# Kernel optimization log

Measured on AMD Instinct MI355X. Metric: run time of the kernel, lower is better.

The kernel has to match this reference:

```python
import jax, jax.numpy as jnp
import numpy as np

TEMPERATURE = 2.0  # registered buffer in the torch module
TAU = 1.0
N_HEADS = 16


def setup_inputs() -> dict:
    key = jax.random.key(0)
    ks = jax.random.split(key, 8)
    B, S, D, N = 4, 1024, 1024, 4096
    scale = 1.0 / np.sqrt(D)
    return {
        "x": jax.random.normal(ks[0], (B, S, D), jnp.float32),
        "in_proj_w": jax.random.normal(ks[1], (3 * D, D), jnp.float32) * scale,
        "in_proj_b": jnp.zeros((3 * D,), jnp.float32),
        "out_w": jax.random.normal(ks[2], (D, D), jnp.float32) * scale,
        "out_b": jnp.zeros((D,), jnp.float32),
        "aff_w": jax.random.normal(ks[3], (N, D), jnp.float32) * scale,
        "aff_b": jnp.zeros((N,), jnp.float32),
        "k": 256,
    }


def _forward(x, in_proj_w, in_proj_b, out_w, out_b, aff_w, aff_b, k):
    B, S, D = x.shape
    H = N_HEADS
    hd = D // H
    # packed QKV projection (torch nn.MultiheadAttention layout)
    qkv = x @ in_proj_w.T + in_proj_b                      # [B,S,3D]
    q, kk, v = jnp.split(qkv, 3, axis=-1)
    q = q.reshape(B, S, H, hd).transpose(0, 2, 1, 3)       # [B,H,S,hd]
    kk = kk.reshape(B, S, H, hd).transpose(0, 2, 1, 3)
    v = v.reshape(B, S, H, hd).transpose(0, 2, 1, 3)
    scores = jnp.einsum("bhqd,bhkd->bhqk", q, kk) / np.sqrt(hd)
    attn = jax.nn.softmax(scores, axis=-1)                 # [B,H,S,S]
    ctx = jnp.einsum("bhqk,bhkd->bhqd", attn, v)
    ctx = ctx.transpose(0, 2, 1, 3).reshape(B, S, D)
    context = ctx @ out_w.T + out_b                        # [B,S,D]
    # neuron affinity -> max-pool over sequence
    affinity = context @ aff_w.T + aff_b                   # [B,S,N]
    pooled = affinity.max(axis=1)                          # [B,N]
    logits = pooled / TEMPERATURE
    # eval path of gumbel-softmax-topk: plain softmax(logits / tau)
    soft = jax.nn.softmax(logits / TAU, axis=-1)
    _, idx = jax.lax.top_k(logits, k)                      # [B,k]
    mask = jnp.zeros_like(soft).at[jnp.arange(soft.shape[0])[:, None], idx].set(1.0)
    masked = soft * mask
    weights = masked / (masked.sum(axis=-1, keepdims=True) + 1e-8)
    return idx, weights, context


def reference(x, in_proj_w, in_proj_b, out_w, out_b, aff_w, aff_b, k):
    return _forward(x, in_proj_w, in_proj_b, out_w, out_b, aff_w, aff_b, k)
```

## Files before the change

kernel.cpp:

```cpp
#include <hip/hip_runtime.h>
#include <math.h>

namespace {

constexpr int Bb = 4, Ss = 1024, Dd = 1024, Hh = 16, HDim = 64, Nn = 4096;
constexpr int Mm = Bb * Ss;

__device__ inline void gload_lds16(const void* g, void* l) {
  __builtin_amdgcn_global_load_lds(
      (const __attribute__((address_space(1))) void*)g,
      (__attribute__((address_space(3))) void*)l, 16, 0, 0);
}

template <int MODE, int TM>
__global__ __launch_bounds__(256, 2) void gemm_f32(
    const float* __restrict__ A, const float* __restrict__ W,
    const float* __restrict__ bias, float* __restrict__ C, const int K,
    const int ldc) {
  constexpr int BM = TM * 16;
  __shared__ float As[2][16][BM];
  __shared__ float Ws[2][16][128];
  __shared__ float red[2][128];
  const int tid = threadIdx.x;
  const int lane = tid & 63, wv = tid >> 6;
  const int wm = wv >> 1, wn = wv & 1;
  const int lty = lane >> 3, ltx = lane & 7;
  const int m0 = blockIdx.y * BM, n0 = blockIdx.x * 128;
  const int row0 = wm * (BM / 2) + lty * TM;
  const int col0 = wn * 64 + ltx * 8;
  const int asrow = (TM == 8) ? (tid >> 1) : (tid >> 2);
  const int asoff = (TM == 8) ? ((tid & 1) * 8) : ((tid & 3) * 4);
  const int bsrow = tid >> 1, bsoff = (tid & 1) * 8;
  const float* Ap = A + (size_t)(m0 + asrow) * K + asoff;
  const float* Wp = W + (size_t)(n0 + bsrow) * K + bsoff;

  float4 a0r, a1r, w0r, w1r;
  a0r = *(const float4*)(Ap);
  if constexpr (TM == 8) a1r = *(const float4*)(Ap + 4);
  w0r = *(const float4*)(Wp);
  w1r = *(const float4*)(Wp + 4);

  float acc[TM][8] = {};
  const int NT = K / 16;
#pragma unroll 1
  for (int kt = 0; kt < NT; ++kt) {
    float* Ab = &As[kt & 1][0][0];
    float* Wb = &Ws[kt & 1][0][0];
    Ab[(asoff + 0) * BM + asrow] = a0r.x;
    Ab[(asoff + 1) * BM + asrow] = a0r.y;
    Ab[(asoff + 2) * BM + asrow] = a0r.z;
    Ab[(asoff + 3) * BM + asrow] = a0r.w;
    if constexpr (TM == 8) {
      Ab[(asoff + 4) * BM + asrow] = a1r.x;
      Ab[(asoff + 5) * BM + asrow] = a1r.y;
      Ab[(asoff + 6) * BM + asrow] = a1r.z;
      Ab[(asoff + 7) * BM + asrow] = a1r.w;
    }
    Wb[(bsoff + 0) * 128 + bsrow] = w0r.x;
    Wb[(bsoff + 1) * 128 + bsrow] = w0r.y;
    Wb[(bsoff + 2) * 128 + bsrow] = w0r.z;
    Wb[(bsoff + 3) * 128 + bsrow] = w0r.w;
    Wb[(bsoff + 4) * 128 + bsrow] = w1r.x;
    Wb[(bsoff + 5) * 128 + bsrow] = w1r.y;
    Wb[(bsoff + 6) * 128 + bsrow] = w1r.z;
    Wb[(bsoff + 7) * 128 + bsrow] = w1r.w;
    __syncthreads();
    if (kt + 1 < NT) {
      const int kb = (kt + 1) * 16;
      a0r = *(const float4*)(Ap + kb);
      if constexpr (TM == 8) a1r = *(const float4*)(Ap + kb + 4);
      w0r = *(const float4*)(Wp + kb);
      w1r = *(const float4*)(Wp + kb + 4);
    }
#pragma unroll
    for (int kk = 0; kk < 16; ++kk) {
      float4 aq0 = *(const float4*)&Ab[kk * BM + row0];
      float4 aq1;
      if constexpr (TM == 8) aq1 = *(const float4*)&Ab[kk * BM + row0 + 4];
      float4 bq0 = *(const float4*)&Wb[kk * 128 + col0];
      float4 bq1 = *(const float4*)&Wb[kk * 128 + col0 + 4];
      float av[TM];
      av[0] = aq0.x; av[1] = aq0.y; av[2] = aq0.z; av[3] = aq0.w;
      if constexpr (TM == 8) {
        av[4] = aq1.x; av[5] = aq1.y; av[6] = aq1.z; av[7] = aq1.w;
      }
      const float bv[8] = {bq0.x, bq0.y, bq0.z, bq0.w,
                           bq1.x, bq1.y, bq1.z, bq1.w};
#pragma unroll
      for (int i = 0; i < TM; ++i)
#pragma unroll
        for (int j = 0; j < 8; ++j)
          acc[i][j] = fmaf(av[i], bv[j], acc[i][j]);
    }
  }

  if constexpr (MODE == 0) {
    float4 bb0 = *(const float4*)&bias[n0 + col0];
    float4 bb1 = *(const float4*)&bias[n0 + col0 + 4];
    const float bvv[8] = {bb0.x, bb0.y, bb0.z, bb0.w,
                          bb1.x, bb1.y, bb1.z, bb1.w};
#pragma unroll
    for (int i = 0; i < TM; ++i) {
      float* crow = C + (size_t)(m0 + row0 + i) * ldc + n0 + col0;
      float4 o0 = {acc[i][0] + bvv[0], acc[i][1] + bvv[1],
                   acc[i][2] + bvv[2], acc[i][3] + bvv[3]};
      float4 o1 = {acc[i][4] + bvv[4], acc[i][5] + bvv[5],
                   acc[i][6] + bvv[6], acc[i][7] + bvv[7]};
      *(float4*)(crow) = o0;
      *(float4*)(crow + 4) = o1;
    }
  } else {
    float cm[8];
#pragma unroll
    for (int j = 0; j < 8; ++j) {
      float m = acc[0][j];
#pragma unroll
      for (int i = 1; i < TM; ++i) m = fmaxf(m, acc[i][j]);
      m = fmaxf(m, __shfl_xor(m, 8));
      m = fmaxf(m, __shfl_xor(m, 16));
      m = fmaxf(m, __shfl_xor(m, 32));
      cm[j] = m;
    }
    __syncthreads();
    if (lty == 0) {
      float4 c0 = {cm[0], cm[1], cm[2], cm[3]};
      float4 c1 = {cm[4], cm[5], cm[6], cm[7]};
      *(float4*)&red[wm][wn * 64 + ltx * 8] = c0;
      *(float4*)&red[wm][wn * 64 + ltx * 8 + 4] = c1;
    }
    __syncthreads();
    if (tid < 128)
      C[(size_t)blockIdx.y * ldc + n0 + tid] =
          fmaxf(red[0][tid], red[1][tid]);
  }
}

__device__ __forceinline__ int kkey(int r) { return ((r >> 3) ^ r) & 7; }
__device__ __forceinline__ int swz(int r, int c) { return c ^ (kkey(r) << 2); }
__device__ __forceinline__ int swzp(int r, int c) {
  return c ^ ((kkey(r) & 3) << 2);
}

__global__ __launch_bounds__(256, 2) void attn_kernel(
    const float* __restrict__ qkv, float* __restrict__ ctx) {
  __shared__ float Qs[4][32][64];
  __shared__ float Ks[2][16][64];
  __shared__ float Vs[2][16][64];
  __shared__ float Pw[4][32][16];
  const int tid = threadIdx.x, wv = tid >> 6, lane = tid & 63;
  const int rg = lane >> 3, cg = lane & 7;
  const int id = blockIdx.x;
  const int qb = id >> 6, bh = id & 63;
  const int b = bh >> 4, h = bh & 15;
  const int q0 = qb * 128 + wv * 32;
  const size_t rstride = 3 * Dd;
  const float* qbp = qkv + (size_t)b * Ss * rstride + h * HDim;
  const float* kbp = qbp + Dd;
  const float* vbp = qbp + 2 * Dd;

  {
    const int r = lane >> 1, ch = (lane & 1) * 32;
    const float* qr = qbp + (size_t)(q0 + r) * rstride + ch;
#pragma unroll
    for (int c = 0; c < 32; c += 4)
      *(float4*)&Qs[wv][r][swz(r, ch + c)] = *(const float4*)(qr + c);
  }

  const int srow = lane >> 4;
  const int scol = (lane & 15) * 4;
#define STAGE_KV(KT, BF)                                                      \
  {                                                                           \
    _Pragma("unroll") for (int j = 0; j < 2; ++j) {                           \
      const int g = wv * 2 + j;                                               \
      const int rr = (g & 3) * 4 + srow;                                      \
      const int cc = swz(rr, scol);                                           \
      if (g < 4)                                                              \
        gload_lds16(kbp + (size_t)((KT) + rr) * rstride + cc,                 \
                    &Ks[BF][(g & 3) * 4][0]);                                 \
      else                                                                    \
        gload_lds16(vbp + (size_t)((KT) + rr) * rstride + cc,                 \
                    &Vs[BF][(g & 3) * 4][0]);                                 \
    }                                                                         \
  }

  STAGE_KV(0, 0);
  __syncthreads();

  float O[4][8] = {};
  float mr[4], lr[4];
#pragma unroll
  for (int i = 0; i < 4; ++i) { mr[i] = -INFINITY; lr[i] = 0.f; }

#pragma unroll 1
  for (int t = 0; t < Ss / 16; ++t) {
    const int cur = t & 1;
    if (t + 1 < Ss / 16) STAGE_KV((t + 1) * 16, cur ^ 1);
    float sc[4][2] = {};
#pragma unroll
    for (int d0 = 0; d0 < HDim; d0 += 4) {
      float4 qa[4], kv[2];
#pragma unroll
      for (int i = 0; i < 4; ++i) {
        const int r = rg * 4 + i;
        qa[i] = *(const float4*)&Qs[wv][r][swz(r, d0)];
      }
#pragma unroll
      for (int j = 0; j < 2; ++j) {
        const int r = cg * 2 + j;
        kv[j] = *(const float4*)&Ks[cur][r][swz(r, d0)];
      }
#pragma unroll
      for (int i = 0; i < 4; ++i)
#pragma unroll
        for (int j = 0; j < 2; ++j) {
          sc[i][j] = fmaf(qa[i].x, kv[j].x, sc[i][j]);
          sc[i][j] = fmaf(qa[i].y, kv[j].y, sc[i][j]);
          sc[i][j] = fmaf(qa[i].z, kv[j].z, sc[i][j]);
          sc[i][j] = fmaf(qa[i].w, kv[j].w, sc[i][j]);
        }
    }
#pragma unroll
    for (int i = 0; i < 4; ++i) {
      const float s0 = sc[i][0] * 0.125f, s1 = sc[i][1] * 0.125f;
      float tm = fmaxf(s0, s1);
      tm = fmaxf(tm, __shfl_xor(tm, 1));
      tm = fmaxf(tm, __shfl_xor(tm, 2));
      tm = fmaxf(tm, __shfl_xor(tm, 4));
      const float mnew = fmaxf(mr[i], tm);
      const float p0 = __expf(s0 - mnew), p1 = __expf(s1 - mnew);
      float rs = p0 + p1;
      rs += __shfl_xor(rs, 1);
      rs += __shfl_xor(rs, 2);
      rs += __shfl_xor(rs, 4);
      const float corr = __expf(mr[i] - mnew);
      lr[i] = lr[i] * corr + rs;
      mr[i] = mnew;
#pragma unroll
      for (int c = 0; c < 8; ++c) O[i][c] *= corr;
      const int r = rg * 4 + i;
      float2 pv = {p0, p1};
      *(float2*)&Pw[wv][r][swzp(r, cg * 2)] = pv;
    }
#pragma unroll
    for (int k0 = 0; k0 < 16; k0 += 4) {
      float4 pa[4];
#pragma unroll
      for (int i = 0; i < 4; ++i) {
        const int r = rg * 4 + i;
        pa[i] = *(const float4*)&Pw[wv][r][swzp(r, k0)];
      }
#pragma unroll
      for (int jj = 0; jj < 4; ++jj) {
        const int vr = k0 + jj;
        const float4 v0 = *(const float4*)&Vs[cur][vr][swz(vr, cg * 8)];
        const float4 v1 = *(const float4*)&Vs[cur][vr][swz(vr, cg * 8 + 4)];
#pragma unroll
        for (int i = 0; i < 4; ++i) {
          const float p = (jj == 0) ? pa[i].x
                          : (jj == 1) ? pa[i].y
                          : (jj == 2) ? pa[i].z : pa[i].w;
          O[i][0] = fmaf(p, v0.x, O[i][0]);
          O[i][1] = fmaf(p, v0.y, O[i][1]);
          O[i][2] = fmaf(p, v0.z, O[i][2]);
          O[i][3] = fmaf(p, v0.w, O[i][3]);
          O[i][4] = fmaf(p, v1.x, O[i][4]);
          O[i][5] = fmaf(p, v1.y, O[i][5]);
          O[i][6] = fmaf(p, v1.z, O[i][6]);
          O[i][7] = fmaf(p, v1.w, O[i][7]);
        }
      }
    }
    __syncthreads();
  }
#pragma unroll
  for (int i = 0; i < 4; ++i) {
    const float inv = 1.0f / lr[i];
    float* orow =
        ctx + ((size_t)(b * Ss + q0 + rg * 4 + i)) * Dd + h * HDim + cg * 8;
    float4 o0 = {O[i][0] * inv, O[i][1] * inv, O[i][2] * inv, O[i][3] * inv};
    float4 o1 = {O[i][4] * inv, O[i][5] * inv, O[i][6] * inv, O[i][7] * inv};
    *(float4*)(orow) = o0;
    *(float4*)(orow + 4) = o1;
  }
#undef STAGE_KV
}

__device__ inline unsigned int f2s(float f) {
  unsigned int u = __float_as_uint(f);
  return (u >> 31) ? ~u : (u | 0x80000000u);
}
__device__ inline float s2f(unsigned int s) {
  unsigned int u = (s >> 31) ? (s & 0x7fffffffu) : ~s;
  return __uint_as_float(u);
}

__global__ __launch_bounds__(256) void router_kernel(
    const float* __restrict__ partial, const float* __restrict__ aff_b,
    const int* __restrict__ kp, float* __restrict__ out, int out_size) {
  __shared__ unsigned long long keys[Nn];
  __shared__ float lorig[Nn];
  __shared__ float rv[4];
  const int tid = threadIdx.x;
  const int b = blockIdx.x;
  const int kcount = *kp;
  float* idx_out = out;
  float* w_out = out + (out_size - Mm * Dd - Bb * Nn);
  for (int n = tid; n < Nn; n += 256) {
    float m = partial[(size_t)(b * 8) * Nn + n];
#pragma unroll
    for (int t = 1; t < 8; ++t)
      m = fmaxf(m, partial[(size_t)(b * 8 + t) * Nn + n]);
    float lg = (m + aff_b[n]) * 0.5f;
    lorig[n] = lg;
    keys[n] = ((unsigned long long)f2s(lg) << 32) | (unsigned int)(Nn - 1 - n);
  }
  __syncthreads();
  for (int kk = 2; kk <= Nn; kk <<= 1) {
    for (int j = kk >> 1; j > 0; j >>= 1) {
#pragma unroll 4
      for (int t = tid; t < Nn / 2; t += 256) {
        const int i = 2 * j * (t / j) + (t % j);
        const int p = i + j;
        const bool desc = ((i & kk) == 0);
        unsigned long long a = keys[i], c = keys[p];
        if (desc ? (a < c) : (a > c)) { keys[i] = c; keys[p] = a; }
      }
      __syncthreads();
    }
  }
  const float gm = s2f((unsigned int)(keys[0] >> 32));
  float se = 0.f;
  for (int n = tid; n < Nn; n += 256) se += expf(lorig[n] - gm);
#pragma unroll
  for (int msk = 1; msk < 64; msk <<= 1) se += __shfl_xor(se, msk);
  if ((tid & 63) == 0) rv[tid >> 6] = se;
  __syncthreads();
  se = rv[0] + rv[1] + rv[2] + rv[3];
  __syncthreads();
  float es = 0.f;
  for (int p = tid; p < kcount; p += 256)
    es += expf(s2f((unsigned int)(keys[p] >> 32)) - gm);
#pragma unroll
  for (int msk = 1; msk < 64; msk <<= 1) es += __shfl_xor(es, msk);
  if ((tid & 63) == 0) rv[tid >> 6] = es;
  __syncthreads();
  es = rv[0] + rv[1] + rv[2] + rv[3];
  const float wd = es / se + 1e-8f;
  for (int n = tid; n < Nn; n += 256) w_out[(size_t)b * Nn + n] = 0.f;
  __syncthreads();
  for (int p = tid; p < kcount; p += 256) {
    const unsigned long long kkey2 = keys[p];
    const int n = Nn - 1 - (int)(kkey2 & 0xffffffffu);
    const float val = s2f((unsigned int)(kkey2 >> 32));
    idx_out[b * kcount + p] = (float)n;
    w_out[(size_t)b * Nn + n] = (expf(val - gm) / se) / wd;
  }
}

}

extern "C" void kernel_launch(void* const* d_in, const int* in_sizes, int n_in,
                              void* d_out, int out_size, void* d_ws,
                              size_t ws_size, hipStream_t stream) {
  (void)in_sizes; (void)n_in; (void)ws_size;
  const float* x = (const float*)d_in[0];
  const float* in_proj_w = (const float*)d_in[1];
  const float* in_proj_b = (const float*)d_in[2];
  const float* out_w = (const float*)d_in[3];
  const float* out_b = (const float*)d_in[4];
  const float* aff_w = (const float*)d_in[5];
  const float* aff_b = (const float*)d_in[6];
  const int* kp = (const int*)d_in[7];

  float* qkv = (float*)d_ws;
  float* ctxws = qkv + (size_t)Mm * 3 * Dd;
  float* partial = ctxws + (size_t)Mm * Dd;

  float* out = (float*)d_out;
  float* ctx_out = out + ((size_t)out_size - (size_t)Mm * Dd);

  gemm_f32<0, 8><<<dim3(3 * Dd / 128, Mm / 128), 256, 0, stream>>>(
      x, in_proj_w, in_proj_b, qkv, Dd, 3 * Dd);
  attn_kernel<<<dim3(Ss / 128 * Bb * Hh), 256, 0, stream>>>(qkv, ctxws);
  gemm_f32<0, 4><<<dim3(Dd / 128, Mm / 64), 256, 0, stream>>>(
      ctxws, out_w, out_b, ctx_out, Dd, Dd);
  gemm_f32<2, 8><<<dim3(Nn / 128, Mm / 128), 256, 0, stream>>>(
      ctx_out, aff_w, nullptr, partial, Dd, Nn);
  router_kernel<<<dim3(Bb), 256, 0, stream>>>(partial, aff_b, kp, out, out_size);
}
```

Before: 1.262 ms.

## Enlarge FP32 GEMM tiles to 256x128 with 16x8 thread microtiles

Replaces the 8-row microtile variant with a 16-row one, giving 256x128 block tiles for the QKV and affinity GEMMs. Each thread now computes a 16x8 outer product per k-step, reading A rows in two split halves 64 apart to limit LDS bank conflicts. The aim is more FMA reuse per shared-memory load. Launch bounds drop to one block per CU-slot, the grid is halved, and the router reduces over 4 partial-max rows instead of 8. In exchange, register pressure and LDS use go up, occupancy goes down, and fewer blocks may leave some CUs underused.

```diff
diff --git a/kernel.cpp b/kernel.cpp
--- a/kernel.cpp
+++ b/kernel.cpp
@@ -13,7 +13,7 @@
 }
 
 template <int MODE, int TM>
-__global__ __launch_bounds__(256, 2) void gemm_f32(
+__global__ __launch_bounds__(256, 1) void gemm_f32(
     const float* __restrict__ A, const float* __restrict__ W,
     const float* __restrict__ bias, float* __restrict__ C, const int K,
     const int ldc) {
@@ -26,17 +26,21 @@
   const int wm = wv >> 1, wn = wv & 1;
   const int lty = lane >> 3, ltx = lane & 7;
   const int m0 = blockIdx.y * BM, n0 = blockIdx.x * 128;
-  const int row0 = wm * (BM / 2) + lty * TM;
+  const int row0 = wm * (BM / 2) + lty * ((TM == 16) ? 8 : TM);
   const int col0 = wn * 64 + ltx * 8;
-  const int asrow = (TM == 8) ? (tid >> 1) : (tid >> 2);
-  const int asoff = (TM == 8) ? ((tid & 1) * 8) : ((tid & 3) * 4);
+  const int asrow = (TM == 16) ? tid : (tid >> 2);
+  const int asoff = (TM == 16) ? 0 : ((tid & 3) * 4);
   const int bsrow = tid >> 1, bsoff = (tid & 1) * 8;
   const float* Ap = A + (size_t)(m0 + asrow) * K + asoff;
   const float* Wp = W + (size_t)(n0 + bsrow) * K + bsoff;
 
-  float4 a0r, a1r, w0r, w1r;
-  a0r = *(const float4*)(Ap);
-  if constexpr (TM == 8) a1r = *(const float4*)(Ap + 4);
+  float4 ar[4], w0r, w1r;
+  ar[0] = *(const float4*)(Ap);
+  if constexpr (TM == 16) {
+    ar[1] = *(const float4*)(Ap + 4);
+    ar[2] = *(const float4*)(Ap + 8);
+    ar[3] = *(const float4*)(Ap + 12);
+  }
   w0r = *(const float4*)(Wp);
   w1r = *(const float4*)(Wp + 4);
 
@@ -46,15 +50,15 @@
   for (int kt = 0; kt < NT; ++kt) {
     float* Ab = &As[kt & 1][0][0];
     float* Wb = &Ws[kt & 1][0][0];
-    Ab[(asoff + 0) * BM + asrow] = a0r.x;
-    Ab[(asoff + 1) * BM + asrow] = a0r.y;
-    Ab[(asoff + 2) * BM + asrow] = a0r.z;
-    Ab[(asoff + 3) * BM + asrow] = a0r.w;
-    if constexpr (TM == 8) {
-      Ab[(asoff + 4) * BM + asrow] = a1r.x;
-      Ab[(asoff + 5) * BM + asrow] = a1r.y;
-      Ab[(asoff + 6) * BM + asrow] = a1r.z;
-      Ab[(asoff + 7) * BM + asrow] = a1r.w;
+    if constexpr (TM == 16) {
+#pragma unroll
+      for (int c = 0; c < 16; ++c)
+        Ab[c * BM + asrow] = ((const float*)ar)[c];
+    } else {
+      Ab[(asoff + 0) * BM + asrow] = ar[0].x;
+      Ab[(asoff + 1) * BM + asrow] = ar[0].y;
+      Ab[(asoff + 2) * BM + asrow] = ar[0].z;
+      Ab[(asoff + 3) * BM + asrow] = ar[0].w;
     }
     Wb[(bsoff + 0) * 128 + bsrow] = w0r.x;
     Wb[(bsoff + 1) * 128 + bsrow] = w0r.y;
@@ -67,23 +71,32 @@
     __syncthreads();
     if (kt + 1 < NT) {
       const int kb = (kt + 1) * 16;
-      a0r = *(const float4*)(Ap + kb);
-      if constexpr (TM == 8) a1r = *(const float4*)(Ap + kb + 4);
+      ar[0] = *(const float4*)(Ap + kb);
+      if constexpr (TM == 16) {
+        ar[1] = *(const float4*)(Ap + kb + 4);
+        ar[2] = *(const float4*)(Ap + kb + 8);
+        ar[3] = *(const float4*)(Ap + kb + 12);
+      }
       w0r = *(const float4*)(Wp + kb);
       w1r = *(const float4*)(Wp + kb + 4);
     }
 #pragma unroll
     for (int kk = 0; kk < 16; ++kk) {
-      float4 aq0 = *(const float4*)&Ab[kk * BM + row0];
-      float4 aq1;
-      if constexpr (TM == 8) aq1 = *(const float4*)&Ab[kk * BM + row0 + 4];
+      float av[TM];
+      {
+        float4 aq0 = *(const float4*)&Ab[kk * BM + row0];
+        av[0] = aq0.x; av[1] = aq0.y; av[2] = aq0.z; av[3] = aq0.w;
+      }
+      if constexpr (TM == 16) {
+        float4 aq1 = *(const float4*)&Ab[kk * BM + row0 + 4];
+        float4 aq2 = *(const float4*)&Ab[kk * BM + row0 + 64];
+        float4 aq3 = *(const float4*)&Ab[kk * BM + row0 + 68];
+        av[4] = aq1.x; av[5] = aq1.y; av[6] = aq1.z; av[7] = aq1.w;
+        av[8] = aq2.x; av[9] = aq2.y; av[10] = aq2.z; av[11] = aq2.w;
+        av[12] = aq3.x; av[13] = aq3.y; av[14] = aq3.z; av[15] = aq3.w;
+      }
       float4 bq0 = *(const float4*)&Wb[kk * 128 + col0];
       float4 bq1 = *(const float4*)&Wb[kk * 128 + col0 + 4];
-      float av[TM];
-      av[0] = aq0.x; av[1] = aq0.y; av[2] = aq0.z; av[3] = aq0.w;
-      if constexpr (TM == 8) {
-        av[4] = aq1.x; av[5] = aq1.y; av[6] = aq1.z; av[7] = aq1.w;
-      }
       const float bv[8] = {bq0.x, bq0.y, bq0.z, bq0.w,
                            bq1.x, bq1.y, bq1.z, bq1.w};
 #pragma unroll
@@ -101,7 +114,8 @@
                           bb1.x, bb1.y, bb1.z, bb1.w};
 #pragma unroll
     for (int i = 0; i < TM; ++i) {
-      float* crow = C + (size_t)(m0 + row0 + i) * ldc + n0 + col0;
+      const int roff = (TM == 16) ? ((i & 7) + (i >> 3) * 64) : i;
+      float* crow = C + (size_t)(m0 + row0 + roff) * ldc + n0 + col0;
       float4 o0 = {acc[i][0] + bvv[0], acc[i][1] + bvv[1],
                    acc[i][2] + bvv[2], acc[i][3] + bvv[3]};
       float4 o1 = {acc[i][4] + bvv[4], acc[i][5] + bvv[5],
@@ -306,10 +320,10 @@
   float* idx_out = out;
   float* w_out = out + (out_size - Mm * Dd - Bb * Nn);
   for (int n = tid; n < Nn; n += 256) {
-    float m = partial[(size_t)(b * 8) * Nn + n];
-#pragma unroll
-    for (int t = 1; t < 8; ++t)
-      m = fmaxf(m, partial[(size_t)(b * 8 + t) * Nn + n]);
+    float m = partial[(size_t)(b * 4) * Nn + n];
+#pragma unroll
+    for (int t = 1; t < 4; ++t)
+      m = fmaxf(m, partial[(size_t)(b * 4 + t) * Nn + n]);
     float lg = (m + aff_b[n]) * 0.5f;
     lorig[n] = lg;
     keys[n] = ((unsigned long long)f2s(lg) << 32) | (unsigned int)(Nn - 1 - n);
@@ -379,12 +393,12 @@
   float* out = (float*)d_out;
   float* ctx_out = out + ((size_t)out_size - (size_t)Mm * Dd);
 
-  gemm_f32<0, 8><<<dim3(3 * Dd / 128, Mm / 128), 256, 0, stream>>>(
+  gemm_f32<0, 16><<<dim3(3 * Dd / 128, Mm / 256), 256, 0, stream>>>(
       x, in_proj_w, in_proj_b, qkv, Dd, 3 * Dd);
   attn_kernel<<<dim3(Ss / 128 * Bb * Hh), 256, 0, stream>>>(qkv, ctxws);
   gemm_f32<0, 4><<<dim3(Dd / 128, Mm / 64), 256, 0, stream>>>(
       ctxws, out_w, out_b, ctx_out, Dd, Dd);
-  gemm_f32<2, 8><<<dim3(Nn / 128, Mm / 128), 256, 0, stream>>>(
+  gemm_f32<2, 16><<<dim3(Nn / 128, Mm / 256), 256, 0, stream>>>(
       ctx_out, aff_w, nullptr, partial, Dd, Nn);
   router_kernel<<<dim3(Bb), 256, 0, stream>>>(partial, aff_b, kp, out, out_size);
 }
```

Result: slower. 1.398 ms (+10.8%).
